# Kernel optimization log

Measured on AMD Instinct MI355X. Metric: run time of the kernel, lower is better.

## Reference

```python
import jax, jax.numpy as jnp
import numpy as np

B, IN, OUT, M = 4096, 512, 512, 16


def setup_inputs() -> dict:
    key = jax.random.key(0)
    k1, k2, k3 = jax.random.split(key, 3)
    # inputs kept strictly positive and inside the physical range [0, 60]
    x = jax.random.uniform(k1, (B, IN), jnp.float32, 0.1, 10.0)
    # photonic basis coefficients: positive, with small polynomial terms
    b_coef = jax.random.uniform(k2, (M, 8), jnp.float32, 0.1, 0.9)
    b_coef = b_coef.at[:, 4:].multiply(0.01)
    coeffs = 0.01 * jax.random.normal(k3, (OUT, IN, M), jnp.float32)
    return {"x": x, "coeffs": coeffs, "b_coef": b_coef}


def _photonic_basis(x, b):
    # x: (B, IN) -> broadcast against M basis functions -> (B, IN, M)
    xe = x[:, :, None]                                   # (B, IN, 1)
    b1, b2, b3, b4, b5, b6, b7, b8 = [b[:, i][None, None, :] for i in range(8)]
    inner = jnp.expm1(b3 * xe)
    powered = jnp.power(inner, b4)
    y = (b1 * jnp.log(1.0 + b2 * jnp.log1p(powered))
         + b5 * xe + b6 * xe**2 + b7 * xe**3 + b8 * xe**4)
    return y


def reference(x, coeffs, b_coef):
    # basis: (B, IN, M); double reduce over (IN, M) == GEMM of size B x (IN*M) x OUT
    basis = _photonic_basis(x, b_coef)
    y = jnp.einsum('bim,oim->bo', basis, coeffs)         # (B, OUT)
    return y
```

## Files before the change

kernel.cpp:

```cpp
#include <hip/hip_runtime.h>
#include <hip/hip_bf16.h>
#include <stdint.h>

#define B_DIM   4096
#define IN_DIM  512
#define OUT_DIM 512
#define M_DIM   16
#define K_DIM   (IN_DIM * M_DIM)
#define MN      (B_DIM * OUT_DIM)

typedef unsigned short ushort_t;
typedef __attribute__((ext_vector_type(8))) __bf16 bf16x8;
typedef __attribute__((ext_vector_type(4))) float  f32x4;

__device__ __forceinline__ ushort_t f2bf(float f) {
  union { float f; uint32_t u; } v; v.f = f;
  uint32_t u = v.u + 0x7fffu + ((v.u >> 16) & 1u);
  return (ushort_t)(u >> 16);
}

#define CONV_N4      (OUT_DIM * K_DIM / 4)
#define CONV_BLOCKS  (CONV_N4 / 256)
#define BASIS_BLOCKS (B_DIM * IN_DIM / 256)

__global__ __launch_bounds__(256) void prep_kernel(
    const float* __restrict__ coeffs, ushort_t* __restrict__ coefb,
    const float* __restrict__ x, const float* __restrict__ bc,
    ushort_t* __restrict__ basis) {
  const int blk = blockIdx.x;
  const int tid = threadIdx.x;
  if (blk < CONV_BLOCKS) {
    int i = blk * 256 + tid;
    float4 v = ((const float4*)coeffs)[i];
    ushort4 o;
    o.x = f2bf(v.x); o.y = f2bf(v.y); o.z = f2bf(v.z); o.w = f2bf(v.w);
    ((ushort4*)coefb)[i] = o;
    return;
  }
  int idx = (blk - CONV_BLOCKS) * 256 + tid;
  float xv = x[idx];
  float x2 = xv * xv, x3 = x2 * xv, x4 = x2 * x2;
  const float LOG2E = 1.44269504088896340736f;
  const float LN2   = 0.69314718055994530942f;
  uint32_t w[8];
  #pragma unroll
  for (int m = 0; m < 16; ++m) {
    float b1 = bc[m*8+0], b2 = bc[m*8+1], b3 = bc[m*8+2], b4 = bc[m*8+3];
    float b5 = bc[m*8+4], b6 = bc[m*8+5], b7 = bc[m*8+6], b8 = bc[m*8+7];
    float e     = __builtin_amdgcn_exp2f(b3 * xv * LOG2E);
    float inner = e - 1.0f;
    float p     = __builtin_amdgcn_exp2f(b4 * __builtin_amdgcn_logf(inner));
    float u     = LN2 * __builtin_amdgcn_logf(1.0f + p);
    float vv    = LN2 * __builtin_amdgcn_logf(1.0f + b2 * u);
    float y = b1 * vv + b5 * xv + b6 * x2 + b7 * x3 + b8 * x4;
    uint32_t h = (uint32_t)f2bf(y);
    if (m & 1) w[m >> 1] |= (h << 16); else w[m >> 1] = h;
  }
  uint4* dst = (uint4*)(basis + (size_t)idx * 16);
  dst[0] = make_uint4(w[0], w[1], w[2], w[3]);
  dst[1] = make_uint4(w[4], w[5], w[6], w[7]);
}

#define BM 128
#define BN 128
#define BK 32
#define SPLITK 8
#define KC (K_DIM / SPLITK)
#define NITER (KC / BK)

#define GLD16(g, l) \
  __builtin_amdgcn_global_load_lds((const __attribute__((address_space(1))) void*)(g), \
                                   (__attribute__((address_space(3))) void*)(l), 16, 0, 0)

template <int ATOMIC>
__global__ __launch_bounds__(256, 4) void gemm_kernel(
    const ushort_t* __restrict__ A,
    const ushort_t* __restrict__ Bt,
    float* __restrict__ P) {
  __shared__ __align__(16) ushort_t As[2][BM * BK];
  __shared__ __align__(16) ushort_t Bs[2][BN * BK];
  const int tid  = threadIdx.x;
  const int wave = tid >> 6;
  const int lane = tid & 63;
  const int bm = blockIdx.x, bn = blockIdx.y, ks = blockIdx.z;

  const int srow = wave * 16 + (lane >> 2);
  const int scol = (((lane & 3) ^ ((lane >> 3) & 3)) * 8);
  const ushort_t* Ag  = A  + (size_t)(bm * BM + srow) * K_DIM + (size_t)ks * KC + scol;
  const ushort_t* Bg  = Bt + (size_t)(bn * BN + srow) * K_DIM + (size_t)ks * KC + scol;
  const ushort_t* Ag2 = Ag + (size_t)64 * K_DIM;
  const ushort_t* Bg2 = Bg + (size_t)64 * K_DIM;
  const int lofs  = wave * 16 * BK;
  const int lofs2 = (wave * 16 + 64) * BK;

#define STAGE(b) do { \
    GLD16(Ag,  &As[b][lofs]);  GLD16(Ag2, &As[b][lofs2]); \
    GLD16(Bg,  &Bs[b][lofs]);  GLD16(Bg2, &Bs[b][lofs2]); \
    Ag += BK; Ag2 += BK; Bg += BK; Bg2 += BK; } while (0)

  const int wr = wave >> 1, wc = wave & 1;
  const int fm = lane & 15;
  const int fkswz = (((lane >> 4) ^ ((lane >> 1) & 3)) << 3);

  f32x4 acc[4][4] = {};

#define COMPUTE(b) do { \
    bf16x8 af[4], bfv[4]; \
    _Pragma("unroll") \
    for (int t = 0; t < 4; ++t) { \
      af[t]  = *(const bf16x8*)&As[b][(wr * 64 + t * 16 + fm) * BK + fkswz]; \
      bfv[t] = *(const bf16x8*)&Bs[b][(wc * 64 + t * 16 + fm) * BK + fkswz]; \
    } \
    _Pragma("unroll") \
    for (int mt = 0; mt < 4; ++mt) \
      _Pragma("unroll") \
      for (int nt = 0; nt < 4; ++nt) \
        acc[mt][nt] = __builtin_amdgcn_mfma_f32_16x16x32_bf16(af[mt], bfv[nt], acc[mt][nt], 0, 0, 0); \
  } while (0)

  STAGE(0);
  for (int kt = 0; kt < NITER - 2; kt += 2) {
    __syncthreads();
    STAGE(1);
    COMPUTE(0);
    __syncthreads();
    STAGE(0);
    COMPUTE(1);
  }
  __syncthreads();
  STAGE(1);
  COMPUTE(0);
  __syncthreads();
  COMPUTE(1);

  const int colb = bn * BN + wc * 64 + fm;
  const int rowb = bm * BM + wr * 64 + (lane >> 4) * 4;
  float* out = P + (ATOMIC ? (size_t)0 : (size_t)ks * MN);
  #pragma unroll
  for (int mt = 0; mt < 4; ++mt) {
    #pragma unroll
    for (int nt = 0; nt < 4; ++nt) {
      #pragma unroll
      for (int j = 0; j < 4; ++j) {
        int row = rowb + mt * 16 + j;
        int col = colb + nt * 16;
        float vv = acc[mt][nt][j];
        if (ATOMIC) atomicAdd(out + (size_t)row * OUT_DIM + col, vv);
        else        out[(size_t)row * OUT_DIM + col] = vv;
      }
    }
  }
#undef STAGE
#undef COMPUTE
}

__global__ __launch_bounds__(256) void reduce_kernel(
    const float* __restrict__ P, float* __restrict__ out) {
  int i = blockIdx.x * 256 + threadIdx.x;
  const float4* p = (const float4*)P;
  float4 r = p[i];
  #pragma unroll
  for (int s = 1; s < SPLITK; ++s) {
    float4 v = p[i + (size_t)s * (MN / 4)];
    r.x += v.x; r.y += v.y; r.z += v.z; r.w += v.w;
  }
  ((float4*)out)[i] = r;
}

extern "C" void kernel_launch(void* const* d_in, const int* in_sizes, int n_in,
                              void* d_out, int out_size, void* d_ws, size_t ws_size,
                              hipStream_t stream) {
  const float* x      = (const float*)d_in[0];
  const float* coeffs = (const float*)d_in[1];
  const float* b_coef = (const float*)d_in[2];
  float* out = (float*)d_out;
  char*  ws  = (char*)d_ws;

  const size_t BASIS_BYTES = (size_t)B_DIM * K_DIM * 2;
  const size_t COEF_BYTES  = (size_t)OUT_DIM * K_DIM * 2;
  ushort_t* basis = (ushort_t*)ws;
  ushort_t* coefb = (ushort_t*)(ws + BASIS_BYTES);
  float* partials = (float*)(ws + BASIS_BYTES + COEF_BYTES);
  const size_t FULL = BASIS_BYTES + COEF_BYTES + (size_t)SPLITK * MN * 4;
  const bool use_atomic = (ws_size < FULL);

  prep_kernel<<<CONV_BLOCKS + BASIS_BLOCKS, 256, 0, stream>>>(
      coeffs, coefb, x, b_coef, basis);

  dim3 grid(B_DIM / BM, OUT_DIM / BN, SPLITK);
  if (use_atomic) {
    hipMemsetAsync(d_out, 0, (size_t)MN * 4, stream);
    gemm_kernel<1><<<grid, 256, 0, stream>>>(basis, coefb, out);
  } else {
    gemm_kernel<0><<<grid, 256, 0, stream>>>(basis, coefb, partials);
    reduce_kernel<<<MN / 4 / 256, 256, 0, stream>>>(partials, out);
  }
}
```

Before: 147.7 us.

## Fuse basis computation into GEMM A-tile staging with full-N 512-thread blocks

Removes the separate basis materialization pass. Each GEMM block now computes the bf16 photonic basis values for its A tile directly into shared memory while the B tile streams in. Blocks now cover all 512 output columns with 8 waves, so each basis element is computed exactly once. This avoids writing and re-reading a 64MB basis buffer. In exchange the GEMM inner loop carries heavy transcendental work, and the larger per-block accumulators and grid reshape to 256 blocks may reduce occupancy and overlap.

```diff
diff --git a/kernel.cpp b/kernel.cpp
--- a/kernel.cpp
+++ b/kernel.cpp
@@ -19,50 +19,24 @@
   return (ushort_t)(u >> 16);
 }
 
-#define CONV_N4      (OUT_DIM * K_DIM / 4)
-#define CONV_BLOCKS  (CONV_N4 / 256)
-#define BASIS_BLOCKS (B_DIM * IN_DIM / 256)
-
-__global__ __launch_bounds__(256) void prep_kernel(
-    const float* __restrict__ coeffs, ushort_t* __restrict__ coefb,
-    const float* __restrict__ x, const float* __restrict__ bc,
-    ushort_t* __restrict__ basis) {
-  const int blk = blockIdx.x;
-  const int tid = threadIdx.x;
-  if (blk < CONV_BLOCKS) {
-    int i = blk * 256 + tid;
-    float4 v = ((const float4*)coeffs)[i];
-    ushort4 o;
-    o.x = f2bf(v.x); o.y = f2bf(v.y); o.z = f2bf(v.z); o.w = f2bf(v.w);
-    ((ushort4*)coefb)[i] = o;
-    return;
-  }
-  int idx = (blk - CONV_BLOCKS) * 256 + tid;
-  float xv = x[idx];
-  float x2 = xv * xv, x3 = x2 * xv, x4 = x2 * x2;
-  const float LOG2E = 1.44269504088896340736f;
-  const float LN2   = 0.69314718055994530942f;
-  uint32_t w[8];
-  #pragma unroll
-  for (int m = 0; m < 16; ++m) {
-    float b1 = bc[m*8+0], b2 = bc[m*8+1], b3 = bc[m*8+2], b4 = bc[m*8+3];
-    float b5 = bc[m*8+4], b6 = bc[m*8+5], b7 = bc[m*8+6], b8 = bc[m*8+7];
-    float e     = __builtin_amdgcn_exp2f(b3 * xv * LOG2E);
-    float inner = e - 1.0f;
-    float p     = __builtin_amdgcn_exp2f(b4 * __builtin_amdgcn_logf(inner));
-    float u     = LN2 * __builtin_amdgcn_logf(1.0f + p);
-    float vv    = LN2 * __builtin_amdgcn_logf(1.0f + b2 * u);
-    float y = b1 * vv + b5 * xv + b6 * x2 + b7 * x3 + b8 * x4;
-    uint32_t h = (uint32_t)f2bf(y);
-    if (m & 1) w[m >> 1] |= (h << 16); else w[m >> 1] = h;
-  }
-  uint4* dst = (uint4*)(basis + (size_t)idx * 16);
-  dst[0] = make_uint4(w[0], w[1], w[2], w[3]);
-  dst[1] = make_uint4(w[4], w[5], w[6], w[7]);
+__device__ __forceinline__ float rfl(float f) {
+  union { float f; int i; } v; v.f = f;
+  v.i = __builtin_amdgcn_readfirstlane(v.i);
+  return v.f;
+}
+
+#define CONV_N4 (OUT_DIM * K_DIM / 4)
+__global__ __launch_bounds__(256) void convert_coeffs_kernel(
+    const float* __restrict__ src, ushort_t* __restrict__ dst) {
+  int i = blockIdx.x * 256 + threadIdx.x;
+  float4 v = ((const float4*)src)[i];
+  ushort4 o;
+  o.x = f2bf(v.x); o.y = f2bf(v.y); o.z = f2bf(v.z); o.w = f2bf(v.w);
+  ((ushort4*)dst)[i] = o;
 }
 
 #define BM 128
-#define BN 128
+#define BN 512
 #define BK 32
 #define SPLITK 8
 #define KC (K_DIM / SPLITK)
@@ -73,73 +47,115 @@
                                    (__attribute__((address_space(3))) void*)(l), 16, 0, 0)
 
 template <int ATOMIC>
-__global__ __launch_bounds__(256, 4) void gemm_kernel(
-    const ushort_t* __restrict__ A,
+__global__ __launch_bounds__(512, 2) void gemm_kernel(
+    const float* __restrict__ x,
     const ushort_t* __restrict__ Bt,
+    const float* __restrict__ bc,
     float* __restrict__ P) {
   __shared__ __align__(16) ushort_t As[2][BM * BK];
   __shared__ __align__(16) ushort_t Bs[2][BN * BK];
   const int tid  = threadIdx.x;
   const int wave = tid >> 6;
   const int lane = tid & 63;
-  const int bm = blockIdx.x, bn = blockIdx.y, ks = blockIdx.z;
+  const int wgid = blockIdx.x;
+  const int ks = wgid & 7, bm = wgid >> 3;
 
   const int srow = wave * 16 + (lane >> 2);
   const int scol = (((lane & 3) ^ ((lane >> 3) & 3)) * 8);
-  const ushort_t* Ag  = A  + (size_t)(bm * BM + srow) * K_DIM + (size_t)ks * KC + scol;
-  const ushort_t* Bg  = Bt + (size_t)(bn * BN + srow) * K_DIM + (size_t)ks * KC + scol;
-  const ushort_t* Ag2 = Ag + (size_t)64 * K_DIM;
-  const ushort_t* Bg2 = Bg + (size_t)64 * K_DIM;
-  const int lofs  = wave * 16 * BK;
-  const int lofs2 = (wave * 16 + 64) * BK;
-
-#define STAGE(b) do { \
-    GLD16(Ag,  &As[b][lofs]);  GLD16(Ag2, &As[b][lofs2]); \
-    GLD16(Bg,  &Bs[b][lofs]);  GLD16(Bg2, &Bs[b][lofs2]); \
-    Ag += BK; Ag2 += BK; Bg += BK; Bg2 += BK; } while (0)
-
-  const int wr = wave >> 1, wc = wave & 1;
+  const ushort_t* Bg0 = Bt + (size_t)srow * K_DIM + ks * KC + scol;
+  const ushort_t* Bg1 = Bg0 + (size_t)128 * K_DIM;
+  const ushort_t* Bg2 = Bg0 + (size_t)256 * K_DIM;
+  const ushort_t* Bg3 = Bg0 + (size_t)384 * K_DIM;
+  const int bofs0 = (wave * 16) * BK;
+  const int bofs1 = (128 + wave * 16) * BK;
+  const int bofs2 = (256 + wave * 16) * BK;
+  const int bofs3 = (384 + wave * 16) * BK;
+
+#define STAGEB(b) do { \
+    GLD16(Bg0, &Bs[b][bofs0]); GLD16(Bg1, &Bs[b][bofs1]); \
+    GLD16(Bg2, &Bs[b][bofs2]); GLD16(Bg3, &Bs[b][bofs3]); \
+    Bg0 += BK; Bg1 += BK; Bg2 += BK; Bg3 += BK; } while (0)
+
+  const int half = wave & 1;
+  const int arow = (wave >> 1) * 32 + (lane >> 1);
+  const int il   = lane & 1;
+  const int aslot = ((il * 2 + half) ^ ((lane >> 2) & 3));
+  const int awe   = arow * BK + aslot * 8;
+  const float* xq = x + (size_t)(bm * BM + arow) * IN_DIM + ks * (KC / M_DIM) + il;
+
+  float c1[8], c2[8], c3[8], c4[8], c5[8], c6[8], c7[8], c8[8];
+  {
+    const float* bch = bc + half * 64;
+    #pragma unroll
+    for (int m = 0; m < 8; ++m) {
+      c1[m] = rfl(bch[m*8+0]); c2[m] = rfl(bch[m*8+1]);
+      c3[m] = rfl(bch[m*8+2]); c4[m] = rfl(bch[m*8+3]);
+      c5[m] = rfl(bch[m*8+4]); c6[m] = rfl(bch[m*8+5]);
+      c7[m] = rfl(bch[m*8+6]); c8[m] = rfl(bch[m*8+7]);
+    }
+  }
+
+  const float LOG2E = 1.44269504088896340736f;
+  const float LN2   = 0.69314718055994530942f;
+#define BASIS(b, t) do { \
+    float xv = xq[(t) * 2]; \
+    float xl2 = xv * LOG2E; \
+    float x2 = xv * xv, x3 = x2 * xv, x4 = x2 * x2; \
+    uint32_t wd[4]; \
+    _Pragma("unroll") \
+    for (int mi = 0; mi < 8; ++mi) { \
+      float e     = __builtin_amdgcn_exp2f(c3[mi] * xl2); \
+      float inner = e - 1.0f; \
+      float p     = __builtin_amdgcn_exp2f(c4[mi] * __builtin_amdgcn_logf(inner)); \
+      float u     = LN2 * __builtin_amdgcn_logf(1.0f + p); \
+      float vv    = LN2 * __builtin_amdgcn_logf(1.0f + c2[mi] * u); \
+      float y = c1[mi] * vv + c5[mi] * xv + c6[mi] * x2 + c7[mi] * x3 + c8[mi] * x4; \
+      uint32_t h = (uint32_t)f2bf(y); \
+      if (mi & 1) wd[mi >> 1] |= (h << 16); else wd[mi >> 1] = h; \
+    } \
+    *(uint4*)&As[b][awe] = make_uint4(wd[0], wd[1], wd[2], wd[3]); \
+  } while (0)
+
+  const int wr = wave >> 2, wc = wave & 3;
   const int fm = lane & 15;
   const int fkswz = (((lane >> 4) ^ ((lane >> 1) & 3)) << 3);
 
-  f32x4 acc[4][4] = {};
+  f32x4 acc[4][8] = {};
 
 #define COMPUTE(b) do { \
-    bf16x8 af[4], bfv[4]; \
-    _Pragma("unroll") \
-    for (int t = 0; t < 4; ++t) { \
-      af[t]  = *(const bf16x8*)&As[b][(wr * 64 + t * 16 + fm) * BK + fkswz]; \
-      bfv[t] = *(const bf16x8*)&Bs[b][(wc * 64 + t * 16 + fm) * BK + fkswz]; \
-    } \
+    bf16x8 af[4], bfv[8]; \
+    _Pragma("unroll") \
+    for (int t2 = 0; t2 < 4; ++t2) \
+      af[t2] = *(const bf16x8*)&As[b][(wr * 64 + t2 * 16 + fm) * BK + fkswz]; \
+    _Pragma("unroll") \
+    for (int u = 0; u < 8; ++u) \
+      bfv[u] = *(const bf16x8*)&Bs[b][(wc * 128 + u * 16 + fm) * BK + fkswz]; \
     _Pragma("unroll") \
     for (int mt = 0; mt < 4; ++mt) \
       _Pragma("unroll") \
-      for (int nt = 0; nt < 4; ++nt) \
+      for (int nt = 0; nt < 8; ++nt) \
         acc[mt][nt] = __builtin_amdgcn_mfma_f32_16x16x32_bf16(af[mt], bfv[nt], acc[mt][nt], 0, 0, 0); \
   } while (0)
 
-  STAGE(0);
+  STAGEB(0); BASIS(0, 0);
+  __syncthreads();
   for (int kt = 0; kt < NITER - 2; kt += 2) {
+    STAGEB(1); COMPUTE(0); BASIS(1, kt + 1);
     __syncthreads();
-    STAGE(1);
-    COMPUTE(0);
+    STAGEB(0); COMPUTE(1); BASIS(0, kt + 2);
     __syncthreads();
-    STAGE(0);
-    COMPUTE(1);
-  }
-  __syncthreads();
-  STAGE(1);
-  COMPUTE(0);
+  }
+  STAGEB(1); COMPUTE(0); BASIS(1, NITER - 1);
   __syncthreads();
   COMPUTE(1);
 
-  const int colb = bn * BN + wc * 64 + fm;
+  const int colb = wc * 128 + fm;
   const int rowb = bm * BM + wr * 64 + (lane >> 4) * 4;
   float* out = P + (ATOMIC ? (size_t)0 : (size_t)ks * MN);
   #pragma unroll
   for (int mt = 0; mt < 4; ++mt) {
     #pragma unroll
-    for (int nt = 0; nt < 4; ++nt) {
+    for (int nt = 0; nt < 8; ++nt) {
       #pragma unroll
       for (int j = 0; j < 4; ++j) {
         int row = rowb + mt * 16 + j;
@@ -150,7 +166,8 @@
       }
     }
   }
-#undef STAGE
+#undef STAGEB
+#undef BASIS
 #undef COMPUTE
 }
 
@@ -176,23 +193,20 @@
   float* out = (float*)d_out;
   char*  ws  = (char*)d_ws;
 
-  const size_t BASIS_BYTES = (size_t)B_DIM * K_DIM * 2;
-  const size_t COEF_BYTES  = (size_t)OUT_DIM * K_DIM * 2;
-  ushort_t* basis = (ushort_t*)ws;
-  ushort_t* coefb = (ushort_t*)(ws + BASIS_BYTES);
-  float* partials = (float*)(ws + BASIS_BYTES + COEF_BYTES);
-  const size_t FULL = BASIS_BYTES + COEF_BYTES + (size_t)SPLITK * MN * 4;
+  const size_t COEF_BYTES = (size_t)OUT_DIM * K_DIM * 2;
+  ushort_t* coefb = (ushort_t*)ws;
+  float* partials = (float*)(ws + COEF_BYTES);
+  const size_t FULL = COEF_BYTES + (size_t)SPLITK * MN * 4;
   const bool use_atomic = (ws_size < FULL);
 
-  prep_kernel<<<CONV_BLOCKS + BASIS_BLOCKS, 256, 0, stream>>>(
-      coeffs, coefb, x, b_coef, basis);
-
-  dim3 grid(B_DIM / BM, OUT_DIM / BN, SPLITK);
+  convert_coeffs_kernel<<<CONV_N4 / 256, 256, 0, stream>>>(coeffs, coefb);
+
+  const int nblk = (B_DIM / BM) * SPLITK;
   if (use_atomic) {
     hipMemsetAsync(d_out, 0, (size_t)MN * 4, stream);
-    gemm_kernel<1><<<grid, 256, 0, stream>>>(basis, coefb, out);
+    gemm_kernel<1><<<nblk, 512, 0, stream>>>(x, coefb, b_coef, out);
   } else {
-    gemm_kernel<0><<<grid, 256, 0, stream>>>(basis, coefb, partials);
+    gemm_kernel<0><<<nblk, 512, 0, stream>>>(x, coefb, b_coef, partials);
     reduce_kernel<<<MN / 4 / 256, 256, 0, stream>>>(partials, out);
   }
 }
```

Measured after the change: 142.9 us. 1.03x faster.
